# Optimization experiments

Hardware: AMD Instinct MI355X
Metric: run time of the kernel (lower is better)

The kernel has to match this reference:

```python
import jax, jax.numpy as jnp
import numpy as np

DIM = 1024
KEY = 128
UV = 1024  # dim * mlp_ratio // 2
SCALE = 1.0 / np.sqrt(KEY).astype(np.float32)
NEG_INF = 1e12


def _sinusoidal(n, d):
    # RoPE tables: sin/cos of shape [n, d//2]
    pos = np.arange(n)[:, None].astype(np.float32)
    inv = (1.0 / 10000 ** (np.arange(0, d, 2).astype(np.float32) / d))[None, :]
    ang = pos * inv
    return jnp.asarray(np.sin(ang)), jnp.asarray(np.cos(ang))


def setup_inputs() -> dict:
    key = jax.random.key(0)
    ks = jax.random.split(key, 4)
    B, N = 4, 2048
    hidden_states = jax.random.normal(ks[0], (B, N, DIM), dtype=jnp.float32)
    attention_mask = jax.random.randint(ks[1], (B, N, N), 0, 2).astype(jnp.int32)
    sin, cos = _sinusoidal(N, KEY)
    Wi = jax.random.normal(ks[2], (DIM, UV * 2 + KEY), dtype=jnp.float32) * (DIM ** -0.5)
    bi = jnp.zeros((UV * 2 + KEY,), jnp.float32)
    Wo = jax.random.normal(ks[3], (UV, DIM), dtype=jnp.float32) * (UV ** -0.5)
    bo = jnp.zeros((DIM,), jnp.float32)
    return {
        "hidden_states": hidden_states, "attention_mask": attention_mask,
        "sin": sin, "cos": cos, "Wi": Wi, "bi": bi, "Wo": Wo, "bo": bo,
        "q_gamma": jnp.ones((KEY,), jnp.float32), "q_beta": jnp.zeros((KEY,), jnp.float32),
        "k_gamma": jnp.ones((KEY,), jnp.float32), "k_beta": jnp.zeros((KEY,), jnp.float32),
    }


def _rotary(x, sin, cos):
    # x: [b, n, d]; sin/cos: [n, d//2]; interleaved RoPE, concat layout
    x1, x2 = x[..., 0::2], x[..., 1::2]
    return jnp.concatenate([x1 * cos - x2 * sin, x1 * sin + x2 * cos], axis=-1)


def reference(hidden_states, attention_mask, sin, cos, Wi, bi, Wo, bo,
              q_gamma, q_beta, k_gamma, k_beta):
    x = jax.nn.silu(hidden_states @ Wi + bi)            # [b, n, 2176]
    u, v, qk = x[..., :UV], x[..., UV:2 * UV], x[..., 2 * UV:]
    q = _rotary(qk * q_gamma + q_beta, sin, cos)        # [b, n, 128]
    k = _rotary(qk * k_gamma + k_beta, sin, cos)
    a = jnp.einsum('bmd,bnd->bmn', q, k) * SCALE        # [b, m, n]
    mask = attention_mask != 0
    a = jnp.where(mask, a, -NEG_INF)
    ll = attention_mask.sum(-1, keepdims=True).astype(a.dtype)  # [b, m, 1]
    A = jnp.square(jax.nn.relu(a)) / ll                 # squared_relu normalize
    out = (u * jnp.einsum('bmn,bnd->bmd', A, v)) @ Wo + bo
    return out
```

## Files before the change

### kernel.cpp

```cpp
#include <hip/hip_runtime.h>
#include <hip/hip_bf16.h>
#include <cstdint>

#define DIM   1024
#define KEY   128
#define UV    1024
#define NCOL  (UV*2 + KEY)
#define SEQ   2048
#define BATCH 4
#define MTOT  (BATCH*SEQ)
#define SCALE 0.08838834764831845f

typedef __attribute__((ext_vector_type(8))) short short8;
typedef __attribute__((ext_vector_type(4))) float f32x4;

__device__ inline unsigned short f2b(float x) {
  unsigned int u = __float_as_uint(x);
  unsigned int r = (u + 0x7fffu + ((u >> 16) & 1u)) >> 16;
  return (unsigned short)r;
}
__device__ inline float b2f(unsigned short x) {
  return __uint_as_float(((unsigned int)x) << 16);
}

__device__ inline void gload_lds16(const void* g, void* l) {
  __builtin_amdgcn_global_load_lds(
      (const __attribute__((address_space(1))) unsigned int*)g,
      (__attribute__((address_space(3))) unsigned int*)l, 16, 0, 0);
}

__device__ inline void mfma_tile_bt(const unsigned short* __restrict__ A,
                                    const unsigned short* __restrict__ Bt,
                                    int K, f32x4 acc[4][4],
                                    unsigned short* ldsA, unsigned short* ldsB) {
  const int tid  = threadIdx.x;
  const int lane = tid & 63;
  const int wid  = tid >> 6;
  const int wr   = wid >> 1, wc = wid & 1;
  const int fr   = lane & 15;
  const int fq   = lane >> 4;

#pragma unroll
  for (int i = 0; i < 4; ++i)
#pragma unroll
    for (int j = 0; j < 4; ++j) acc[i][j] = (f32x4){0.f, 0.f, 0.f, 0.f};

  for (int k0 = 0; k0 < K; k0 += 32) {
    __syncthreads();
#pragma unroll
    for (int i = 0; i < 2; ++i) {
      int c   = i * 256 + tid;
      int row = c >> 2;
      int kc  = (c & 3) * 8;
      int basechunk = i * 256 + wid * 64;
      gload_lds16(A  + (size_t)row * K + k0 + kc, ldsA + (size_t)basechunk * 8);
      gload_lds16(Bt + (size_t)row * K + k0 + kc, ldsB + (size_t)basechunk * 8);
    }
    __syncthreads();

    short8 af[4], bf[4];
#pragma unroll
    for (int s = 0; s < 4; ++s) {
      af[s] = *(const short8*)&ldsA[(wr * 64 + s * 16 + fr) * 32 + fq * 8];
      bf[s] = *(const short8*)&ldsB[(wc * 64 + s * 16 + fr) * 32 + fq * 8];
    }
#pragma unroll
    for (int i = 0; i < 4; ++i)
#pragma unroll
      for (int j = 0; j < 4; ++j)
        acc[i][j] = __builtin_amdgcn_mfma_f32_16x16x32_bf16(af[i], bf[j], acc[i][j], 0, 0, 0);
  }
}

#define EPILOGUE_COORDS()                      \
  const int lane = threadIdx.x & 63;           \
  const int wid  = threadIdx.x >> 6;           \
  const int wr   = wid >> 1, wc = wid & 1;     \
  const int fr   = lane & 15;                  \
  const int fq   = lane >> 4;

__global__ __launch_bounds__(256) void k_cvt(const float* __restrict__ in,
                                             unsigned short* __restrict__ out) {
  int id = blockIdx.x * 256 + threadIdx.x;
  float4 f = ((const float4*)in)[id];
  ushort4 o;
  o.x = f2b(f.x); o.y = f2b(f.y); o.z = f2b(f.z); o.w = f2b(f.w);
  ((ushort4*)out)[id] = o;
}

__global__ void k_tcvt(const float* __restrict__ in, unsigned short* __restrict__ out,
                       int R, int C) {
  __shared__ float t[32][33];
  int c0 = blockIdx.x * 32, r0 = blockIdx.y * 32;
  int tx = threadIdx.x, ty = threadIdx.y;
#pragma unroll
  for (int i = 0; i < 4; ++i)
    t[ty + i * 8][tx] = in[(size_t)(r0 + ty + i * 8) * C + c0 + tx];
  __syncthreads();
#pragma unroll
  for (int i = 0; i < 4; ++i)
    out[(size_t)(c0 + ty + i * 8) * R + r0 + tx] = f2b(t[tx][ty + i * 8]);
}

__global__ __launch_bounds__(256) void k_masksum(const int* __restrict__ mask,
                                                 float* __restrict__ ll) {
  int wid = threadIdx.x >> 6, lane = threadIdx.x & 63;
  int row = blockIdx.x * 4 + wid;
  const int4* p = (const int4*)(mask + (size_t)row * SEQ);
  int s = 0;
#pragma unroll
  for (int i = 0; i < 8; ++i) { int4 v = p[lane + 64 * i]; s += v.x + v.y + v.z + v.w; }
  for (int off = 32; off; off >>= 1) s += __shfl_down(s, off);
  if (lane == 0) ll[row] = (float)s;
}

__global__ __launch_bounds__(256) void k_rope(const float* __restrict__ qk,
                                              const float* __restrict__ sn,
                                              const float* __restrict__ cs,
                                              const float* __restrict__ qg,
                                              const float* __restrict__ qb,
                                              const float* __restrict__ kg,
                                              const float* __restrict__ kb,
                                              unsigned short* __restrict__ q,
                                              unsigned short* __restrict__ k) {
  int id = blockIdx.x * 256 + threadIdx.x;
  int m = id >> 6, t = id & 63;
  int n = m & (SEQ - 1);
  float x1 = qk[m * KEY + 2 * t], x2 = qk[m * KEY + 2 * t + 1];
  float s_ = sn[n * 64 + t], c_ = cs[n * 64 + t];
  float a1 = x1 * qg[2 * t] + qb[2 * t];
  float a2 = x2 * qg[2 * t + 1] + qb[2 * t + 1];
  q[m * KEY + t]      = f2b(a1 * c_ - a2 * s_);
  q[m * KEY + 64 + t] = f2b(a1 * s_ + a2 * c_);
  float b1 = x1 * kg[2 * t] + kb[2 * t];
  float b2 = x2 * kg[2 * t + 1] + kb[2 * t + 1];
  k[m * KEY + t]      = f2b(b1 * c_ - b2 * s_);
  k[m * KEY + 64 + t] = f2b(b1 * s_ + b2 * c_);
}

__global__ __launch_bounds__(256) void k_vT(const unsigned short* __restrict__ v,
                                            unsigned short* __restrict__ vT) {
  __shared__ unsigned short t[64][65];
  int b = blockIdx.z;
  int n0 = blockIdx.x * 64;
  int d0 = blockIdx.y * 64;
  int tid = threadIdx.x;
  int r = tid >> 4;
  int c4 = (tid & 15) * 4;
#pragma unroll
  for (int i = 0; i < 4; ++i) {
    int n = n0 + r + i * 16;
    ushort4 val = *(const ushort4*)&v[((size_t)b * SEQ + n) * UV + d0 + c4];
    t[c4 + 0][r + i * 16] = val.x;
    t[c4 + 1][r + i * 16] = val.y;
    t[c4 + 2][r + i * 16] = val.z;
    t[c4 + 3][r + i * 16] = val.w;
  }
  __syncthreads();
#pragma unroll
  for (int i = 0; i < 4; ++i) {
    int d = d0 + r + i * 16;
    ushort4 o;
    o.x = t[r + i * 16][c4 + 0];
    o.y = t[r + i * 16][c4 + 1];
    o.z = t[r + i * 16][c4 + 2];
    o.w = t[r + i * 16][c4 + 3];
    *(ushort4*)&vT[((size_t)b * UV + d) * SEQ + n0 + c4] = o;
  }
}

__global__ __launch_bounds__(256) void k_gemm1(const unsigned short* __restrict__ hbf,
                                               const unsigned short* __restrict__ WiT,
                                               const float* __restrict__ bi,
                                               unsigned short* __restrict__ u,
                                               unsigned short* __restrict__ v,
                                               float* __restrict__ qk) {
  __shared__ unsigned short ldsA[128 * 32], ldsB[128 * 32];
  int m0 = blockIdx.x * 128, n0 = blockIdx.y * 128;
  f32x4 acc[4][4];
  mfma_tile_bt(hbf + (size_t)m0 * DIM, WiT + (size_t)n0 * DIM, DIM, acc, ldsA, ldsB);
  EPILOGUE_COORDS();
#pragma unroll
  for (int i = 0; i < 4; ++i)
#pragma unroll
    for (int j = 0; j < 4; ++j)
#pragma unroll
      for (int r = 0; r < 4; ++r) {
        int row = m0 + wr * 64 + i * 16 + fq * 4 + r;
        int col = n0 + wc * 64 + j * 16 + fr;
        float x = acc[i][j][r] + bi[col];
        float s = x / (1.f + __expf(-x));
        if (col < UV)            u[(size_t)row * UV + col] = f2b(s);
        else if (col < 2 * UV)   v[(size_t)row * UV + col - UV] = f2b(s);
        else                     qk[(size_t)row * KEY + col - 2 * UV] = s;
      }
}

__global__ __launch_bounds__(256) void k_qk(const unsigned short* __restrict__ q,
                                            const unsigned short* __restrict__ k,
                                            const int* __restrict__ mask,
                                            const float* __restrict__ ll,
                                            unsigned short* __restrict__ Abuf) {
  __shared__ unsigned short ldsA[128 * 32], ldsB[128 * 32];
  int b = blockIdx.z;
  int m0 = blockIdx.x * 128, n0 = blockIdx.y * 128;
  f32x4 acc[4][4];
  mfma_tile_bt(q + ((size_t)b * SEQ + m0) * KEY, k + ((size_t)b * SEQ + n0) * KEY,
               KEY, acc, ldsA, ldsB);
  EPILOGUE_COORDS();
#pragma unroll
  for (int i = 0; i < 4; ++i)
#pragma unroll
    for (int j = 0; j < 4; ++j)
#pragma unroll
      for (int r = 0; r < 4; ++r) {
        int row = m0 + wr * 64 + i * 16 + fq * 4 + r;
        int col = n0 + wc * 64 + j * 16 + fr;
        float a = acc[i][j][r] * SCALE;
        int mk = mask[((size_t)b * SEQ + row) * SEQ + col];
        float rel = (mk != 0 && a > 0.f) ? a : 0.f;
        float Av = rel * rel / ll[b * SEQ + row];
        Abuf[((size_t)b * SEQ + row) * SEQ + col] = f2b(Av);
      }
}

__global__ __launch_bounds__(256) void k_av(const unsigned short* __restrict__ Abuf,
                                            const unsigned short* __restrict__ vT,
                                            const unsigned short* __restrict__ u,
                                            unsigned short* __restrict__ g) {
  __shared__ unsigned short ldsA[128 * 32], ldsB[128 * 32];
  int b = blockIdx.z;
  int m0 = blockIdx.x * 128, n0 = blockIdx.y * 128;
  f32x4 acc[4][4];
  mfma_tile_bt(Abuf + ((size_t)b * SEQ + m0) * SEQ, vT + ((size_t)b * UV + n0) * SEQ,
               SEQ, acc, ldsA, ldsB);
  EPILOGUE_COORDS();
#pragma unroll
  for (int i = 0; i < 4; ++i)
#pragma unroll
    for (int j = 0; j < 4; ++j)
#pragma unroll
      for (int r = 0; r < 4; ++r) {
        int row = m0 + wr * 64 + i * 16 + fq * 4 + r;
        int col = n0 + wc * 64 + j * 16 + fr;
        size_t gi = ((size_t)b * SEQ + row) * UV + col;
        g[gi] = f2b(acc[i][j][r] * b2f(u[gi]));
      }
}

__global__ __launch_bounds__(256) void k_out(const unsigned short* __restrict__ g,
                                             const unsigned short* __restrict__ WoT,
                                             const float* __restrict__ bo,
                                             float* __restrict__ out) {
  __shared__ unsigned short ldsA[128 * 32], ldsB[128 * 32];
  int m0 = blockIdx.x * 128, n0 = blockIdx.y * 128;
  f32x4 acc[4][4];
  mfma_tile_bt(g + (size_t)m0 * UV, WoT + (size_t)n0 * UV, UV, acc, ldsA, ldsB);
  EPILOGUE_COORDS();
#pragma unroll
  for (int i = 0; i < 4; ++i)
#pragma unroll
    for (int j = 0; j < 4; ++j)
#pragma unroll
      for (int r = 0; r < 4; ++r) {
        int row = m0 + wr * 64 + i * 16 + fq * 4 + r;
        int col = n0 + wc * 64 + j * 16 + fr;
        out[(size_t)row * DIM + col] = acc[i][j][r] + bo[col];
      }
}

extern "C" void kernel_launch(void* const* d_in, const int* in_sizes, int n_in,
                              void* d_out, int out_size, void* d_ws, size_t ws_size,
                              hipStream_t stream) {
  const float* h    = (const float*)d_in[0];
  const int*   mask = (const int*)d_in[1];
  const float* sn   = (const float*)d_in[2];
  const float* cs   = (const float*)d_in[3];
  const float* Wi   = (const float*)d_in[4];
  const float* bi   = (const float*)d_in[5];
  const float* Wo   = (const float*)d_in[6];
  const float* bo   = (const float*)d_in[7];
  const float* qg   = (const float*)d_in[8];
  const float* qb   = (const float*)d_in[9];
  const float* kg   = (const float*)d_in[10];
  const float* kb   = (const float*)d_in[11];
  float* out = (float*)d_out;

  char* ws = (char*)d_ws;
  size_t off = 0;
  auto alloc = [&](size_t bytes) { void* p = ws + off; off += (bytes + 255) & ~(size_t)255; return p; };
  unsigned short* hbf  = (unsigned short*)alloc((size_t)MTOT * DIM * 2);
  unsigned short* WiT  = (unsigned short*)alloc((size_t)NCOL * DIM * 2);
  unsigned short* WoT  = (unsigned short*)alloc((size_t)DIM * UV * 2);
  unsigned short* u    = (unsigned short*)alloc((size_t)MTOT * UV * 2);
  unsigned short* v    = (unsigned short*)alloc((size_t)MTOT * UV * 2);
  unsigned short* vT   = (unsigned short*)alloc((size_t)MTOT * UV * 2);
  float*          qkb  = (float*)alloc((size_t)MTOT * KEY * 4);
  unsigned short* qbuf = (unsigned short*)alloc((size_t)MTOT * KEY * 2);
  unsigned short* kbuf = (unsigned short*)alloc((size_t)MTOT * KEY * 2);
  float*          ll   = (float*)alloc((size_t)MTOT * 4);
  unsigned short* Abuf = (unsigned short*)alloc((size_t)BATCH * SEQ * SEQ * 2);
  unsigned short* g    = (unsigned short*)alloc((size_t)MTOT * UV * 2);

  k_cvt<<<(MTOT * DIM / 4) / 256, 256, 0, stream>>>(h, hbf);
  k_tcvt<<<dim3(NCOL / 32, DIM / 32), dim3(32, 8), 0, stream>>>(Wi, WiT, DIM, NCOL);
  k_tcvt<<<dim3(UV / 32, DIM / 32), dim3(32, 8), 0, stream>>>(Wo, WoT, DIM, UV);
  k_masksum<<<MTOT / 4, 256, 0, stream>>>(mask, ll);

  k_gemm1<<<dim3(MTOT / 128, NCOL / 128), 256, 0, stream>>>(hbf, WiT, bi, u, v, qkb);
  k_rope<<<(MTOT * 64) / 256, 256, 0, stream>>>(qkb, sn, cs, qg, qb, kg, kb, qbuf, kbuf);
  k_vT<<<dim3(SEQ / 64, UV / 64, BATCH), 256, 0, stream>>>(v, vT);
  k_qk<<<dim3(SEQ / 128, SEQ / 128, BATCH), 256, 0, stream>>>(qbuf, kbuf, mask, ll, Abuf);
  k_av<<<dim3(SEQ / 128, UV / 128, BATCH), 256, 0, stream>>>(Abuf, vT, u, g);
  k_out<<<dim3(MTOT / 128, DIM / 128), 256, 0, stream>>>(g, WoT, bo, out);
}
```

Before: 208.3 us.

## Replace GEMM core with 256x128 eight-wave triple-buffered swizzled MFMA pipeline

The shared GEMM helper is rewritten to use 256x128 tiles with 512 threads (8 waves) and K steps of 64. Global-to-LDS loads go into three rotating buffers two steps ahead, governed by vmcnt waits instead of full syncthreads. LDS chunks are XOR-swizzled to reduce bank conflicts, and s_setprio is raised around the MFMA bursts. All four GEMM kernels use it with 144KB of dynamic LDS, which limits each CU to one block and halves the grid sizes, so occupancy and tail balance may suffer.

```diff
diff --git a/kernel.cpp b/kernel.cpp
--- a/kernel.cpp
+++ b/kernel.cpp
@@ -29,53 +29,105 @@
       (__attribute__((address_space(3))) unsigned int*)l, 16, 0, 0);
 }
 
-__device__ inline void mfma_tile_bt(const unsigned short* __restrict__ A,
-                                    const unsigned short* __restrict__ Bt,
-                                    int K, f32x4 acc[4][4],
-                                    unsigned short* ldsA, unsigned short* ldsB) {
+__device__ __forceinline__ void gemm8w_256x128(
+    const unsigned short* __restrict__ A, int lda,
+    const unsigned short* __restrict__ Bt, int ldb,
+    int K, f32x4 acc[4][4], unsigned short* lds) {
   const int tid  = threadIdx.x;
   const int lane = tid & 63;
   const int wid  = tid >> 6;
-  const int wr   = wid >> 1, wc = wid & 1;
+  const int wm   = wid >> 1;
+  const int wn   = wid & 1;
   const int fr   = lane & 15;
   const int fq   = lane >> 4;
 
+  unsigned short* ldsA = lds;
+  unsigned short* ldsB = lds + 3 * 16384;
+
 #pragma unroll
   for (int i = 0; i < 4; ++i)
 #pragma unroll
     for (int j = 0; j < 4; ++j) acc[i][j] = (f32x4){0.f, 0.f, 0.f, 0.f};
 
-  for (int k0 = 0; k0 < K; k0 += 32) {
-    __syncthreads();
-#pragma unroll
-    for (int i = 0; i < 2; ++i) {
-      int c   = i * 256 + tid;
-      int row = c >> 2;
-      int kc  = (c & 3) * 8;
-      int basechunk = i * 256 + wid * 64;
-      gload_lds16(A  + (size_t)row * K + k0 + kc, ldsA + (size_t)basechunk * 8);
-      gload_lds16(Bt + (size_t)row * K + k0 + kc, ldsB + (size_t)basechunk * 8);
+  auto stage = [&](int t, int b) {
+    const unsigned short* Ag = A + (size_t)t * 64;
+    const unsigned short* Bg = Bt + (size_t)t * 64;
+    unsigned short* la = ldsA + b * 16384;
+    unsigned short* lb = ldsB + b * 8192;
+#pragma unroll
+    for (int p = 0; p < 4; ++p) {
+      int c = p * 512 + tid, r = c >> 3, q = c & 7;
+      int qs = q ^ ((r >> 2) & 3);
+      gload_lds16(Ag + (size_t)r * lda + qs * 8, la + ((size_t)(p * 512 + wid * 64)) * 8);
     }
-    __syncthreads();
+#pragma unroll
+    for (int p = 0; p < 2; ++p) {
+      int c = p * 512 + tid, r = c >> 3, q = c & 7;
+      int qs = q ^ ((r >> 2) & 3);
+      gload_lds16(Bg + (size_t)r * ldb + qs * 8, lb + ((size_t)(p * 512 + wid * 64)) * 8);
+    }
+  };
+
+  const int swz   = (fr >> 2) & 3;
+  const int colk0 = (fq ^ swz) * 8;
+  const int rA    = (wm * 64 + fr) * 64;
+  const int rB    = (wn * 64 + fr) * 64;
+
+  const int NT = K >> 6;
+  stage(0, 0);
+  stage(1, 1);
+  asm volatile("s_waitcnt vmcnt(6)" ::: "memory");
+  __builtin_amdgcn_s_barrier();
+  asm volatile("" ::: "memory");
+
+  int cur = 0;
+  for (int t = 0; t < NT; ++t) {
+    unsigned short* la = ldsA + cur * 16384;
+    unsigned short* lb = ldsB + cur * 8192;
+    const int c2 = (cur >= 1) ? cur - 1 : 2;
+    const bool more = (t + 2) < NT;
+    if (more) stage(t + 2, c2);
 
     short8 af[4], bf[4];
 #pragma unroll
-    for (int s = 0; s < 4; ++s) {
-      af[s] = *(const short8*)&ldsA[(wr * 64 + s * 16 + fr) * 32 + fq * 8];
-      bf[s] = *(const short8*)&ldsB[(wc * 64 + s * 16 + fr) * 32 + fq * 8];
-    }
+    for (int i = 0; i < 4; ++i) af[i] = *(const short8*)&la[rA + i * 1024 + colk0];
+#pragma unroll
+    for (int j = 0; j < 4; ++j) bf[j] = *(const short8*)&lb[rB + j * 1024 + colk0];
+    __builtin_amdgcn_s_barrier();
+    asm volatile("" ::: "memory");
+    __builtin_amdgcn_s_setprio(1);
 #pragma unroll
     for (int i = 0; i < 4; ++i)
 #pragma unroll
       for (int j = 0; j < 4; ++j)
         acc[i][j] = __builtin_amdgcn_mfma_f32_16x16x32_bf16(af[i], bf[j], acc[i][j], 0, 0, 0);
+    __builtin_amdgcn_s_setprio(0);
+#pragma unroll
+    for (int i = 0; i < 4; ++i) af[i] = *(const short8*)&la[rA + i * 1024 + colk0 + 32];
+#pragma unroll
+    for (int j = 0; j < 4; ++j) bf[j] = *(const short8*)&lb[rB + j * 1024 + colk0 + 32];
+    __builtin_amdgcn_s_barrier();
+    asm volatile("" ::: "memory");
+    __builtin_amdgcn_s_setprio(1);
+#pragma unroll
+    for (int i = 0; i < 4; ++i)
+#pragma unroll
+      for (int j = 0; j < 4; ++j)
+        acc[i][j] = __builtin_amdgcn_mfma_f32_16x16x32_bf16(af[i], bf[j], acc[i][j], 0, 0, 0);
+    __builtin_amdgcn_s_setprio(0);
+    asm volatile("" ::: "memory");
+    if (more) asm volatile("s_waitcnt vmcnt(6)" ::: "memory");
+    else      asm volatile("s_waitcnt vmcnt(0)" ::: "memory");
+    __builtin_amdgcn_s_barrier();
+    asm volatile("" ::: "memory");
+    cur = (cur == 2) ? 0 : cur + 1;
   }
 }
 
 #define EPILOGUE_COORDS()                      \
   const int lane = threadIdx.x & 63;           \
   const int wid  = threadIdx.x >> 6;           \
-  const int wr   = wid >> 1, wc = wid & 1;     \
+  const int wm   = wid >> 1, wn = wid & 1;     \
   const int fr   = lane & 15;                  \
   const int fq   = lane >> 4;
 
@@ -169,16 +221,18 @@
   }
 }
 
-__global__ __launch_bounds__(256) void k_gemm1(const unsigned short* __restrict__ hbf,
-                                               const unsigned short* __restrict__ WiT,
-                                               const float* __restrict__ bi,
-                                               unsigned short* __restrict__ u,
-                                               unsigned short* __restrict__ v,
-                                               float* __restrict__ qk) {
-  __shared__ unsigned short ldsA[128 * 32], ldsB[128 * 32];
-  int m0 = blockIdx.x * 128, n0 = blockIdx.y * 128;
+#define LDS_BYTES 147456
+
+__global__ __launch_bounds__(512, 2) void k_gemm1(const unsigned short* __restrict__ hbf,
+                                                  const unsigned short* __restrict__ WiT,
+                                                  const float* __restrict__ bi,
+                                                  unsigned short* __restrict__ u,
+                                                  unsigned short* __restrict__ v,
+                                                  float* __restrict__ qk) {
+  extern __shared__ unsigned short lds[];
+  int m0 = blockIdx.x * 256, n0 = blockIdx.y * 128;
   f32x4 acc[4][4];
-  mfma_tile_bt(hbf + (size_t)m0 * DIM, WiT + (size_t)n0 * DIM, DIM, acc, ldsA, ldsB);
+  gemm8w_256x128(hbf + (size_t)m0 * DIM, DIM, WiT + (size_t)n0 * DIM, DIM, DIM, acc, lds);
   EPILOGUE_COORDS();
 #pragma unroll
   for (int i = 0; i < 4; ++i)
@@ -186,27 +240,27 @@
     for (int j = 0; j < 4; ++j)
 #pragma unroll
       for (int r = 0; r < 4; ++r) {
-        int row = m0 + wr * 64 + i * 16 + fq * 4 + r;
-        int col = n0 + wc * 64 + j * 16 + fr;
+        int row = m0 + wm * 64 + i * 16 + fq * 4 + r;
+        int col = n0 + wn * 64 + j * 16 + fr;
         float x = acc[i][j][r] + bi[col];
         float s = x / (1.f + __expf(-x));
-        if (col < UV)            u[(size_t)row * UV + col] = f2b(s);
-        else if (col < 2 * UV)   v[(size_t)row * UV + col - UV] = f2b(s);
-        else                     qk[(size_t)row * KEY + col - 2 * UV] = s;
+        if (n0 < UV)            u[(size_t)row * UV + col] = f2b(s);
+        else if (n0 < 2 * UV)   v[(size_t)row * UV + col - UV] = f2b(s);
+        else                    qk[(size_t)row * KEY + col - 2 * UV] = s;
       }
 }
 
-__global__ __launch_bounds__(256) void k_qk(const unsigned short* __restrict__ q,
-                                            const unsigned short* __restrict__ k,
-                                            const int* __restrict__ mask,
-                                            const float* __restrict__ ll,
-                                            unsigned short* __restrict__ Abuf) {
-  __shared__ unsigned short ldsA[128 * 32], ldsB[128 * 32];
+__global__ __launch_bounds__(512, 2) void k_qk(const unsigned short* __restrict__ q,
+                                               const unsigned short* __restrict__ k,
+                                               const int* __restrict__ mask,
+                                               const float* __restrict__ ll,
+                                               unsigned short* __restrict__ Abuf) {
+  extern __shared__ unsigned short lds[];
   int b = blockIdx.z;
-  int m0 = blockIdx.x * 128, n0 = blockIdx.y * 128;
+  int m0 = blockIdx.x * 256, n0 = blockIdx.y * 128;
   f32x4 acc[4][4];
-  mfma_tile_bt(q + ((size_t)b * SEQ + m0) * KEY, k + ((size_t)b * SEQ + n0) * KEY,
-               KEY, acc, ldsA, ldsB);
+  gemm8w_256x128(q + ((size_t)b * SEQ + m0) * KEY, KEY,
+                 k + ((size_t)b * SEQ + n0) * KEY, KEY, KEY, acc, lds);
   EPILOGUE_COORDS();
 #pragma unroll
   for (int i = 0; i < 4; ++i)
@@ -214,8 +268,8 @@
     for (int j = 0; j < 4; ++j)
 #pragma unroll
       for (int r = 0; r < 4; ++r) {
-        int row = m0 + wr * 64 + i * 16 + fq * 4 + r;
-        int col = n0 + wc * 64 + j * 16 + fr;
+        int row = m0 + wm * 64 + i * 16 + fq * 4 + r;
+        int col = n0 + wn * 64 + j * 16 + fr;
         float a = acc[i][j][r] * SCALE;
         int mk = mask[((size_t)b * SEQ + row) * SEQ + col];
         float rel = (mk != 0 && a > 0.f) ? a : 0.f;
@@ -224,16 +278,16 @@
       }
 }
 
-__global__ __launch_bounds__(256) void k_av(const unsigned short* __restrict__ Abuf,
-                                            const unsigned short* __restrict__ vT,
-                                            const unsigned short* __restrict__ u,
-                                            unsigned short* __restrict__ g) {
-  __shared__ unsigned short ldsA[128 * 32], ldsB[128 * 32];
+__global__ __launch_bounds__(512, 2) void k_av(const unsigned short* __restrict__ Abuf,
+                                               const unsigned short* __restrict__ vT,
+                                               const unsigned short* __restrict__ u,
+                                               unsigned short* __restrict__ g) {
+  extern __shared__ unsigned short lds[];
   int b = blockIdx.z;
-  int m0 = blockIdx.x * 128, n0 = blockIdx.y * 128;
+  int m0 = blockIdx.x * 256, n0 = blockIdx.y * 128;
   f32x4 acc[4][4];
-  mfma_tile_bt(Abuf + ((size_t)b * SEQ + m0) * SEQ, vT + ((size_t)b * UV + n0) * SEQ,
-               SEQ, acc, ldsA, ldsB);
+  gemm8w_256x128(Abuf + ((size_t)b * SEQ + m0) * SEQ, SEQ,
+                 vT + ((size_t)b * UV + n0) * SEQ, SEQ, SEQ, acc, lds);
   EPILOGUE_COORDS();
 #pragma unroll
   for (int i = 0; i < 4; ++i)
@@ -241,21 +295,21 @@
     for (int j = 0; j < 4; ++j)
 #pragma unroll
       for (int r = 0; r < 4; ++r) {
-        int row = m0 + wr * 64 + i * 16 + fq * 4 + r;
-        int col = n0 + wc * 64 + j * 16 + fr;
+        int row = m0 + wm * 64 + i * 16 + fq * 4 + r;
+        int col = n0 + wn * 64 + j * 16 + fr;
         size_t gi = ((size_t)b * SEQ + row) * UV + col;
         g[gi] = f2b(acc[i][j][r] * b2f(u[gi]));
       }
 }
 
-__global__ __launch_bounds__(256) void k_out(const unsigned short* __restrict__ g,
-                                             const unsigned short* __restrict__ WoT,
-                                             const float* __restrict__ bo,
-                                             float* __restrict__ out) {
-  __shared__ unsigned short ldsA[128 * 32], ldsB[128 * 32];
-  int m0 = blockIdx.x * 128, n0 = blockIdx.y * 128;
+__global__ __launch_bounds__(512, 2) void k_out(const unsigned short* __restrict__ g,
+                                                const unsigned short* __restrict__ WoT,
+                                                const float* __restrict__ bo,
+                                                float* __restrict__ out) {
+  extern __shared__ unsigned short lds[];
+  int m0 = blockIdx.x * 256, n0 = blockIdx.y * 128;
   f32x4 acc[4][4];
-  mfma_tile_bt(g + (size_t)m0 * UV, WoT + (size_t)n0 * UV, UV, acc, ldsA, ldsB);
+  gemm8w_256x128(g + (size_t)m0 * UV, UV, WoT + (size_t)n0 * UV, UV, UV, acc, lds);
   EPILOGUE_COORDS();
 #pragma unroll
   for (int i = 0; i < 4; ++i)
@@ -263,8 +317,8 @@
     for (int j = 0; j < 4; ++j)
 #pragma unroll
       for (int r = 0; r < 4; ++r) {
-        int row = m0 + wr * 64 + i * 16 + fq * 4 + r;
-        int col = n0 + wc * 64 + j * 16 + fr;
+        int row = m0 + wm * 64 + i * 16 + fq * 4 + r;
+        int col = n0 + wn * 64 + j * 16 + fr;
         out[(size_t)row * DIM + col] = acc[i][j][r] + bo[col];
       }
 }
@@ -286,6 +340,12 @@
   const float* kb   = (const float*)d_in[11];
   float* out = (float*)d_out;
 
+  static_assert(LDS_BYTES == (3 * 16384 + 3 * 8192) * 2, "lds size");
+  hipFuncSetAttribute((const void*)k_gemm1, hipFuncAttributeMaxDynamicSharedMemorySize, LDS_BYTES);
+  hipFuncSetAttribute((const void*)k_qk,    hipFuncAttributeMaxDynamicSharedMemorySize, LDS_BYTES);
+  hipFuncSetAttribute((const void*)k_av,    hipFuncAttributeMaxDynamicSharedMemorySize, LDS_BYTES);
+  hipFuncSetAttribute((const void*)k_out,   hipFuncAttributeMaxDynamicSharedMemorySize, LDS_BYTES);
+
   char* ws = (char*)d_ws;
   size_t off = 0;
   auto alloc = [&](size_t bytes) { void* p = ws + off; off += (bytes + 255) & ~(size_t)255; return p; };
@@ -307,10 +367,10 @@
   k_tcvt<<<dim3(UV / 32, DIM / 32), dim3(32, 8), 0, stream>>>(Wo, WoT, DIM, UV);
   k_masksum<<<MTOT / 4, 256, 0, stream>>>(mask, ll);
 
-  k_gemm1<<<dim3(MTOT / 128, NCOL / 128), 256, 0, stream>>>(hbf, WiT, bi, u, v, qkb);
+  k_gemm1<<<dim3(MTOT / 256, NCOL / 128), 512, LDS_BYTES, stream>>>(hbf, WiT, bi, u, v, qkb);
   k_rope<<<(MTOT * 64) / 256, 256, 0, stream>>>(qkb, sn, cs, qg, qb, kg, kb, qbuf, kbuf);
   k_vT<<<dim3(SEQ / 64, UV / 64, BATCH), 256, 0, stream>>>(v, vT);
-  k_qk<<<dim3(SEQ / 128, SEQ / 128, BATCH), 256, 0, stream>>>(qbuf, kbuf, mask, ll, Abuf);
-  k_av<<<dim3(SEQ / 128, UV / 128, BATCH), 256, 0, stream>>>(Abuf, vT, u, g);
-  k_out<<<dim3(MTOT / 128, DIM / 128), 256, 0, stream>>>(g, WoT, bo, out);
-}
+  k_qk<<<dim3(SEQ / 256, SEQ / 128, BATCH), 512, LDS_BYTES, stream>>>(qbuf, kbuf, mask, ll, Abuf);
+  k_av<<<dim3(SEQ / 256, UV / 128, BATCH), 512, LDS_BYTES, stream>>>(Abuf, vT, u, g);
+  k_out<<<dim3(MTOT / 256, DIM / 128), 512, LDS_BYTES, stream>>>(g, WoT, bo, out);
+}
```

Measured after the change: 236.9 us. 1.14x slower.

## Double-buffer GEMM LDS with swizzle, XCD remap, and bit-packed attention mask

Applied to the files above, without the earlier changes.

Replaces the shared GEMM loop with a double-buffered version that issues the next k-slice's global-to-LDS loads before computing the current one, and XOR-swizzles LDS chunks to cut bank conflicts. It also remaps block indices across XCDs and raises occupancy bounds. The mask-sum kernel now also emits a bit-packed mask, so the QK epilogue reads 64-bit words instead of the full int32 mask and uses a precomputed reciprocal of the row count. The explicit waitcnt and barrier choreography adds fragility, and the swizzle and remap must stay consistent across all GEMMs.

```diff
diff --git a/kernel.cpp b/kernel.cpp
--- a/kernel.cpp
+++ b/kernel.cpp
@@ -29,10 +29,10 @@
       (__attribute__((address_space(3))) unsigned int*)l, 16, 0, 0);
 }
 
-__device__ inline void mfma_tile_bt(const unsigned short* __restrict__ A,
-                                    const unsigned short* __restrict__ Bt,
-                                    int K, f32x4 acc[4][4],
-                                    unsigned short* ldsA, unsigned short* ldsB) {
+__device__ __forceinline__ void gemm128(
+    const unsigned short* __restrict__ A, int lda,
+    const unsigned short* __restrict__ Bt, int ldb,
+    int K, f32x4 acc[4][4], unsigned short* lds) {
   const int tid  = threadIdx.x;
   const int lane = tid & 63;
   const int wid  = tid >> 6;
@@ -45,30 +45,59 @@
 #pragma unroll
     for (int j = 0; j < 4; ++j) acc[i][j] = (f32x4){0.f, 0.f, 0.f, 0.f};
 
-  for (int k0 = 0; k0 < K; k0 += 32) {
-    __syncthreads();
-#pragma unroll
-    for (int i = 0; i < 2; ++i) {
-      int c   = i * 256 + tid;
-      int row = c >> 2;
-      int kc  = (c & 3) * 8;
-      int basechunk = i * 256 + wid * 64;
-      gload_lds16(A  + (size_t)row * K + k0 + kc, ldsA + (size_t)basechunk * 8);
-      gload_lds16(Bt + (size_t)row * K + k0 + kc, ldsB + (size_t)basechunk * 8);
-    }
-    __syncthreads();
-
+  auto stage = [&](int k, int d) {
+    unsigned short* la = lds + d * 8192;
+    unsigned short* lb = la + 4096;
+#pragma unroll
+    for (int p = 0; p < 2; ++p) {
+      int c = p * 256 + tid;
+      int r = c >> 2, q = c & 3;
+      int qs = q ^ ((r >> 1) & 3);
+      gload_lds16(A + (size_t)r * lda + k * 32 + qs * 8,
+                  la + (size_t)(p * 256 + wid * 64) * 8);
+    }
+#pragma unroll
+    for (int p = 0; p < 2; ++p) {
+      int c = p * 256 + tid;
+      int r = c >> 2, q = c & 3;
+      int qs = q ^ ((r >> 1) & 3);
+      gload_lds16(Bt + (size_t)r * ldb + k * 32 + qs * 8,
+                  lb + (size_t)(p * 256 + wid * 64) * 8);
+    }
+  };
+
+  const int slot = (fq ^ ((fr >> 1) & 3)) * 8;
+  const int rA   = (wr * 64 + fr) * 32 + slot;
+  const int rB   = (wc * 64 + fr) * 32 + slot;
+
+  const int NK = K >> 5;
+  stage(0, 0);
+  for (int k = 0; k < NK; ++k) {
+    const int d = k & 1;
+    if (k + 1 < NK) {
+      stage(k + 1, d ^ 1);
+      asm volatile("s_waitcnt vmcnt(4)" ::: "memory");
+    } else {
+      asm volatile("s_waitcnt vmcnt(0)" ::: "memory");
+    }
+    __builtin_amdgcn_s_barrier();
+    asm volatile("" ::: "memory");
+    const unsigned short* la = lds + d * 8192;
+    const unsigned short* lb = la + 4096;
     short8 af[4], bf[4];
 #pragma unroll
     for (int s = 0; s < 4; ++s) {
-      af[s] = *(const short8*)&ldsA[(wr * 64 + s * 16 + fr) * 32 + fq * 8];
-      bf[s] = *(const short8*)&ldsB[(wc * 64 + s * 16 + fr) * 32 + fq * 8];
+      af[s] = *(const short8*)&la[rA + s * 512];
+      bf[s] = *(const short8*)&lb[rB + s * 512];
     }
 #pragma unroll
     for (int i = 0; i < 4; ++i)
 #pragma unroll
       for (int j = 0; j < 4; ++j)
         acc[i][j] = __builtin_amdgcn_mfma_f32_16x16x32_bf16(af[i], bf[j], acc[i][j], 0, 0, 0);
+    asm volatile("" ::: "memory");
+    __builtin_amdgcn_s_barrier();
+    asm volatile("" ::: "memory");
   }
 }
 
@@ -78,6 +107,15 @@
   const int wr   = wid >> 1, wc = wid & 1;     \
   const int fr   = lane & 15;                  \
   const int fq   = lane >> 4;
+
+__device__ __forceinline__ void xcd_swz(int& tx, int& ty) {
+  const int gx = gridDim.x, gy = gridDim.y;
+  const int n = gx * gy;
+  const int D = blockIdx.y * gx + blockIdx.x;
+  const int c = (D & 7) * (n >> 3) + (D >> 3);
+  tx = c / gy;
+  ty = c - tx * gy;
+}
 
 __global__ __launch_bounds__(256) void k_cvt(const float* __restrict__ in,
                                              unsigned short* __restrict__ out) {
@@ -102,14 +140,25 @@
     out[(size_t)(c0 + ty + i * 8) * R + r0 + tx] = f2b(t[tx][ty + i * 8]);
 }
 
-__global__ __launch_bounds__(256) void k_masksum(const int* __restrict__ mask,
-                                                 float* __restrict__ ll) {
+__global__ __launch_bounds__(256) void k_maskprep(const int* __restrict__ mask,
+                                                  float* __restrict__ ll,
+                                                  unsigned int* __restrict__ mb) {
   int wid = threadIdx.x >> 6, lane = threadIdx.x & 63;
   int row = blockIdx.x * 4 + wid;
   const int4* p = (const int4*)(mask + (size_t)row * SEQ);
   int s = 0;
 #pragma unroll
-  for (int i = 0; i < 8; ++i) { int4 v = p[lane + 64 * i]; s += v.x + v.y + v.z + v.w; }
+  for (int i = 0; i < 8; ++i) {
+    int4 v = p[i * 64 + lane];
+    unsigned nib = (v.x != 0 ? 1u : 0u) | (v.y != 0 ? 2u : 0u) |
+                   (v.z != 0 ? 4u : 0u) | (v.w != 0 ? 8u : 0u);
+    unsigned w = 0;
+#pragma unroll
+    for (int k2 = 0; k2 < 8; ++k2)
+      w |= __shfl(nib, (lane & ~7) + k2, 64) << (4 * k2);
+    if ((lane & 7) == 0) mb[(size_t)row * 64 + i * 8 + (lane >> 3)] = w;
+    s += v.x + v.y + v.z + v.w;
+  }
   for (int off = 32; off; off >>= 1) s += __shfl_down(s, off);
   if (lane == 0) ll[row] = (float)s;
 }
@@ -169,16 +218,17 @@
   }
 }
 
-__global__ __launch_bounds__(256) void k_gemm1(const unsigned short* __restrict__ hbf,
-                                               const unsigned short* __restrict__ WiT,
-                                               const float* __restrict__ bi,
-                                               unsigned short* __restrict__ u,
-                                               unsigned short* __restrict__ v,
-                                               float* __restrict__ qk) {
-  __shared__ unsigned short ldsA[128 * 32], ldsB[128 * 32];
-  int m0 = blockIdx.x * 128, n0 = blockIdx.y * 128;
+__global__ __launch_bounds__(256, 4) void k_gemm1(const unsigned short* __restrict__ hbf,
+                                                  const unsigned short* __restrict__ WiT,
+                                                  const float* __restrict__ bi,
+                                                  unsigned short* __restrict__ u,
+                                                  unsigned short* __restrict__ v,
+                                                  float* __restrict__ qk) {
+  __shared__ unsigned short lds[16384];
+  int tx, ty; xcd_swz(tx, ty);
+  int m0 = tx * 128, n0 = ty * 128;
   f32x4 acc[4][4];
-  mfma_tile_bt(hbf + (size_t)m0 * DIM, WiT + (size_t)n0 * DIM, DIM, acc, ldsA, ldsB);
+  gemm128(hbf + (size_t)m0 * DIM, DIM, WiT + (size_t)n0 * DIM, DIM, DIM, acc, lds);
   EPILOGUE_COORDS();
 #pragma unroll
   for (int i = 0; i < 4; ++i)
@@ -190,50 +240,56 @@
         int col = n0 + wc * 64 + j * 16 + fr;
         float x = acc[i][j][r] + bi[col];
         float s = x / (1.f + __expf(-x));
-        if (col < UV)            u[(size_t)row * UV + col] = f2b(s);
-        else if (col < 2 * UV)   v[(size_t)row * UV + col - UV] = f2b(s);
-        else                     qk[(size_t)row * KEY + col - 2 * UV] = s;
+        if (n0 < UV)            u[(size_t)row * UV + col] = f2b(s);
+        else if (n0 < 2 * UV)   v[(size_t)row * UV + col - UV] = f2b(s);
+        else                    qk[(size_t)row * KEY + col - 2 * UV] = s;
       }
 }
 
-__global__ __launch_bounds__(256) void k_qk(const unsigned short* __restrict__ q,
-                                            const unsigned short* __restrict__ k,
-                                            const int* __restrict__ mask,
-                                            const float* __restrict__ ll,
-                                            unsigned short* __restrict__ Abuf) {
-  __shared__ unsigned short ldsA[128 * 32], ldsB[128 * 32];
+__global__ __launch_bounds__(256, 4) void k_qk(const unsigned short* __restrict__ q,
+                                               const unsigned short* __restrict__ k,
+                                               const unsigned int* __restrict__ mb,
+                                               const float* __restrict__ ll,
+                                               unsigned short* __restrict__ Abuf) {
+  __shared__ unsigned short lds[16384];
   int b = blockIdx.z;
-  int m0 = blockIdx.x * 128, n0 = blockIdx.y * 128;
+  int tx, ty; xcd_swz(tx, ty);
+  int m0 = tx * 128, n0 = ty * 128;
   f32x4 acc[4][4];
-  mfma_tile_bt(q + ((size_t)b * SEQ + m0) * KEY, k + ((size_t)b * SEQ + n0) * KEY,
-               KEY, acc, ldsA, ldsB);
+  gemm128(q + ((size_t)b * SEQ + m0) * KEY, KEY,
+          k + ((size_t)b * SEQ + n0) * KEY, KEY, KEY, acc, lds);
   EPILOGUE_COORDS();
 #pragma unroll
   for (int i = 0; i < 4; ++i)
 #pragma unroll
-    for (int j = 0; j < 4; ++j)
-#pragma unroll
-      for (int r = 0; r < 4; ++r) {
-        int row = m0 + wr * 64 + i * 16 + fq * 4 + r;
+    for (int r = 0; r < 4; ++r) {
+      int row = m0 + wr * 64 + i * 16 + fq * 4 + r;
+      size_t rb = (size_t)b * SEQ + row;
+      unsigned long long mw =
+          *(const unsigned long long*)&mb[rb * 64 + (n0 >> 5) + wc * 2];
+      float rll = 1.0f / ll[rb];
+#pragma unroll
+      for (int j = 0; j < 4; ++j) {
         int col = n0 + wc * 64 + j * 16 + fr;
         float a = acc[i][j][r] * SCALE;
-        int mk = mask[((size_t)b * SEQ + row) * SEQ + col];
-        float rel = (mk != 0 && a > 0.f) ? a : 0.f;
-        float Av = rel * rel / ll[b * SEQ + row];
-        Abuf[((size_t)b * SEQ + row) * SEQ + col] = f2b(Av);
+        bool on = (mw >> (j * 16 + fr)) & 1ull;
+        float rel = (on && a > 0.f) ? a : 0.f;
+        Abuf[rb * SEQ + col] = f2b(rel * rel * rll);
       }
-}
-
-__global__ __launch_bounds__(256) void k_av(const unsigned short* __restrict__ Abuf,
-                                            const unsigned short* __restrict__ vT,
-                                            const unsigned short* __restrict__ u,
-                                            unsigned short* __restrict__ g) {
-  __shared__ unsigned short ldsA[128 * 32], ldsB[128 * 32];
+    }
+}
+
+__global__ __launch_bounds__(256, 4) void k_av(const unsigned short* __restrict__ Abuf,
+                                               const unsigned short* __restrict__ vT,
+                                               const unsigned short* __restrict__ u,
+                                               unsigned short* __restrict__ g) {
+  __shared__ unsigned short lds[16384];
   int b = blockIdx.z;
-  int m0 = blockIdx.x * 128, n0 = blockIdx.y * 128;
+  int tx, ty; xcd_swz(tx, ty);
+  int m0 = tx * 128, n0 = ty * 128;
   f32x4 acc[4][4];
-  mfma_tile_bt(Abuf + ((size_t)b * SEQ + m0) * SEQ, vT + ((size_t)b * UV + n0) * SEQ,
-               SEQ, acc, ldsA, ldsB);
+  gemm128(Abuf + ((size_t)b * SEQ + m0) * SEQ, SEQ,
+          vT + ((size_t)b * UV + n0) * SEQ, SEQ, SEQ, acc, lds);
   EPILOGUE_COORDS();
 #pragma unroll
   for (int i = 0; i < 4; ++i)
@@ -248,14 +304,15 @@
       }
 }
 
-__global__ __launch_bounds__(256) void k_out(const unsigned short* __restrict__ g,
-                                             const unsigned short* __restrict__ WoT,
-                                             const float* __restrict__ bo,
-                                             float* __restrict__ out) {
-  __shared__ unsigned short ldsA[128 * 32], ldsB[128 * 32];
-  int m0 = blockIdx.x * 128, n0 = blockIdx.y * 128;
+__global__ __launch_bounds__(256, 4) void k_out(const unsigned short* __restrict__ g,
+                                                const unsigned short* __restrict__ WoT,
+                                                const float* __restrict__ bo,
+                                                float* __restrict__ out) {
+  __shared__ unsigned short lds[16384];
+  int tx, ty; xcd_swz(tx, ty);
+  int m0 = tx * 128, n0 = ty * 128;
   f32x4 acc[4][4];
-  mfma_tile_bt(g + (size_t)m0 * UV, WoT + (size_t)n0 * UV, UV, acc, ldsA, ldsB);
+  gemm128(g + (size_t)m0 * UV, UV, WoT + (size_t)n0 * UV, UV, UV, acc, lds);
   EPILOGUE_COORDS();
 #pragma unroll
   for (int i = 0; i < 4; ++i)
@@ -299,18 +356,19 @@
   unsigned short* qbuf = (unsigned short*)alloc((size_t)MTOT * KEY * 2);
   unsigned short* kbuf = (unsigned short*)alloc((size_t)MTOT * KEY * 2);
   float*          ll   = (float*)alloc((size_t)MTOT * 4);
+  unsigned int*   mbits= (unsigned int*)alloc((size_t)MTOT * 64 * 4);
   unsigned short* Abuf = (unsigned short*)alloc((size_t)BATCH * SEQ * SEQ * 2);
   unsigned short* g    = (unsigned short*)alloc((size_t)MTOT * UV * 2);
 
   k_cvt<<<(MTOT * DIM / 4) / 256, 256, 0, stream>>>(h, hbf);
   k_tcvt<<<dim3(NCOL / 32, DIM / 32), dim3(32, 8), 0, stream>>>(Wi, WiT, DIM, NCOL);
   k_tcvt<<<dim3(UV / 32, DIM / 32), dim3(32, 8), 0, stream>>>(Wo, WoT, DIM, UV);
-  k_masksum<<<MTOT / 4, 256, 0, stream>>>(mask, ll);
+  k_maskprep<<<MTOT / 4, 256, 0, stream>>>(mask, ll, mbits);
 
   k_gemm1<<<dim3(MTOT / 128, NCOL / 128), 256, 0, stream>>>(hbf, WiT, bi, u, v, qkb);
   k_rope<<<(MTOT * 64) / 256, 256, 0, stream>>>(qkb, sn, cs, qg, qb, kg, kb, qbuf, kbuf);
   k_vT<<<dim3(SEQ / 64, UV / 64, BATCH), 256, 0, stream>>>(v, vT);
-  k_qk<<<dim3(SEQ / 128, SEQ / 128, BATCH), 256, 0, stream>>>(qbuf, kbuf, mask, ll, Abuf);
+  k_qk<<<dim3(SEQ / 128, SEQ / 128, BATCH), 256, 0, stream>>>(qbuf, kbuf, mbits, ll, Abuf);
   k_av<<<dim3(SEQ / 128, UV / 128, BATCH), 256, 0, stream>>>(Abuf, vT, u, g);
   k_out<<<dim3(MTOT / 128, DIM / 128), 256, 0, stream>>>(g, WoT, bo, out);
 }
```

New measurement: 190.2 us. -8.7%, faster.
